# Kernel tuning notes

Hardware: AMD Instinct MI355X
Metric: run time of the kernel (lower is better)

Reference implementation:

```python
import jax, jax.numpy as jnp
import numpy as np

MINIMUM_VALUE = -1e9  # C.MINIMUM_VALUE: large negative fill for masked positions


def setup_inputs() -> dict:
    key = jax.random.key(0)
    kq, kv, km, kw = jax.random.split(key, 4)
    B, N, H = 8, 2048, 1024
    query = jax.random.normal(kq, (B, N, H), dtype=jnp.float32)
    value = jax.random.normal(kv, (B, N, H), dtype=jnp.float32)
    mask = jax.random.randint(km, (B, N, N), 0, 2, dtype=jnp.int32)
    W = jax.random.normal(kw, (H, H), dtype=jnp.float32)
    return {"query": query, "value": value, "mask": mask, "W": W}


def reference(query, value, mask, W):
    # intermediate = query @ W           : B x M x H
    # e = relu(intermediate @ value^T)   : B x M x N
    e = jax.nn.relu(jnp.einsum("bmh,hk,bnk->bmn", query, W, value))
    attn_logits = jnp.where(mask > 0, e, MINIMUM_VALUE)
    attn = jax.nn.softmax(attn_logits, axis=-1)
    output = jnp.einsum("bmn,bnh->bmh", attn, value)
    return (output, attn)
```

## Files before the change

kernel.cpp:

```cpp
#include <hip/hip_runtime.h>


typedef _Float16 half8 __attribute__((ext_vector_type(8)));
typedef float f32x4 __attribute__((ext_vector_type(4)));
typedef unsigned short u16;
typedef unsigned int u32;

#define BATCH 8
#define SEQ   2048
#define HID   1024
#define MINV  (-1e9f)

#define AS1 __attribute__((address_space(1)))
#define AS3 __attribute__((address_space(3)))

__device__ __forceinline__ u16 h2u(_Float16 h) { return __builtin_bit_cast(u16, h); }

__device__ __forceinline__ u32 packhl(float x) {
    _Float16 h = (_Float16)x;
    _Float16 l = (_Float16)(x - (float)h);
    return (u32)h2u(h) | ((u32)h2u(l) << 16);
}

__device__ __forceinline__ void gload16(const char* g, AS3 char* l) {
    __builtin_amdgcn_global_load_lds((const AS1 void*)g, (AS3 void*)l, 16, 0, 0);
}

__global__ __launch_bounds__(256) void prep_v(const float* __restrict__ V,
                                              u16* __restrict__ Vp,
                                              u16* __restrict__ Vt)
{
    __shared__ __align__(16) u16 lt[64 * 72];
    const int b = blockIdx.z, n0 = blockIdx.y * 64, h0 = blockIdx.x * 64;
    const int t = threadIdx.x;
    const int r = t >> 4, c4 = (t & 15) * 4;
#pragma unroll
    for (int it = 0; it < 4; ++it) {
        const int rr = r + it * 16;
        const float4 x = *(const float4*)(V + ((size_t)b * SEQ + n0 + rr) * HID + h0 + c4);
        const float xs[4] = {x.x, x.y, x.z, x.w};
        u32 p[4];
#pragma unroll
        for (int e = 0; e < 4; ++e) {
            p[e] = packhl(xs[e]);
            lt[(c4 + e) * 72 + rr] = (u16)p[e];
        }
        const int g = (h0 + c4) >> 5, j = c4 & 31;
        u16* base = Vp + (((size_t)b * SEQ + n0 + rr) * 32 + g) * 64;
        *(uint2*)(base + j) = make_uint2((p[0] & 0xffffu) | (p[1] << 16),
                                         (p[2] & 0xffffu) | (p[3] << 16));
        *(uint2*)(base + 32 + j) = make_uint2((p[0] >> 16) | (p[1] & 0xffff0000u),
                                              (p[2] >> 16) | (p[3] & 0xffff0000u));
    }
    __syncthreads();
    const int hr = t >> 2, cc = (t & 3) * 2;
    uint4 v0 = *(const uint4*)&lt[hr * 72 + cc * 8];
    uint4 v1 = *(const uint4*)&lt[hr * 72 + cc * 8 + 8];
    u16* dst = Vt + ((size_t)b * HID + h0 + hr) * SEQ + n0 + cc * 8;
    *(uint4*)dst = v0;
    *(uint4*)(dst + 8) = v1;
}

__global__ __launch_bounds__(256) void prep_w(const float* __restrict__ W,
                                              u16* __restrict__ Wtp)
{
    __shared__ __align__(16) u32 lt[64 * 68];
    const int n0 = blockIdx.x * 64, k0 = blockIdx.y * 64;
    const int t = threadIdx.x;
    const int r = t >> 4, c4 = (t & 15) * 4;
#pragma unroll
    for (int it = 0; it < 4; ++it) {
        const int rr = r + it * 16;
        const float4 x = *(const float4*)(W + (size_t)(k0 + rr) * HID + n0 + c4);
        const float xs[4] = {x.x, x.y, x.z, x.w};
#pragma unroll
        for (int e = 0; e < 4; ++e) lt[(c4 + e) * 68 + rr] = packhl(xs[e]);
    }
    __syncthreads();
    const int n = t >> 2;
#pragma unroll
    for (int s = 0; s < 4; ++s) {
        const int ci = (t & 3) + s * 4;
        uint4 v = *(const uint4*)&lt[n * 68 + ci * 4];
        const int k = k0 + ci * 4;
        u16* base = Wtp + (((size_t)n0 + n) * 32 + (k >> 5)) * 64;
        const int j = k & 31;
        *(uint2*)(base + j) = make_uint2((v.x & 0xffffu) | (v.y << 16),
                                         (v.z & 0xffffu) | (v.w << 16));
        *(uint2*)(base + 32 + j) = make_uint2((v.x >> 16) | (v.y & 0xffff0000u),
                                              (v.z >> 16) | (v.w & 0xffff0000u));
    }
}

__global__ __launch_bounds__(256) void prep_q(const float* __restrict__ Q,
                                              u16* __restrict__ Qp)
{
    const size_t row = blockIdx.x;
    const int t = threadIdx.x;
    const float4 x = ((const float4*)(Q + row * HID))[t];
    const u32 p0 = packhl(x.x), p1 = packhl(x.y), p2 = packhl(x.z), p3 = packhl(x.w);
    const int k = t * 4;
    u16* base = Qp + (row * 32 + (k >> 5)) * 64;
    const int j = k & 31;
    *(uint2*)(base + j) = make_uint2((p0 & 0xffffu) | (p1 << 16),
                                     (p2 & 0xffffu) | (p3 << 16));
    *(uint2*)(base + 32 + j) = make_uint2((p0 >> 16) | (p1 & 0xffff0000u),
                                          (p2 >> 16) | (p3 & 0xffff0000u));
}

template <bool SPLIT>
__device__ __forceinline__ void cluster4x2(f32x4 (&acc)[8][4], int ib, int jb,
                                           const half8 (&ah)[4], const half8 (&al)[4],
                                           half8 bh0, half8 bl0, half8 bh1, half8 bl1)
{
#pragma unroll
    for (int f = 0; f < 4; ++f) {
#pragma unroll
        for (int jj = 0; jj < 2; ++jj) {
            const half8 bh = jj ? bh1 : bh0;
            const half8 bl = jj ? bl1 : bl0;
            f32x4 c = acc[ib + f][jb + jj];
            if constexpr (SPLIT) {
                c = __builtin_amdgcn_mfma_f32_16x16x32_f16(al[f], bh, c, 0, 0, 0);
                c = __builtin_amdgcn_mfma_f32_16x16x32_f16(ah[f], bl, c, 0, 0, 0);
                c = __builtin_amdgcn_mfma_f32_16x16x32_f16(ah[f], bh, c, 0, 0, 0);
            } else {
                c = __builtin_amdgcn_mfma_f32_16x16x32_f16(ah[f], bh, c, 0, 0, 0);
                c = __builtin_amdgcn_mfma_f32_16x16x32_f16(al[f], bl, c, 0, 0, 0);
            }
            acc[ib + f][jb + jj] = c;
        }
    }
}

#define SBAR() __builtin_amdgcn_sched_barrier(0)

template <int MODE, int ROT, int CUR>
__device__ __forceinline__ void kstep(
    const char* pAh, const char* pAl, const char* pBh, const char* pBl,
    AS3 char* lds,
    const char* __restrict__ Ab, const char* __restrict__ Bb,
    const u32 (&aoffs)[4], const u32 (&boffs)[4], const int (&dsto)[4],
    u32 kb, bool more, f32x4 (&acc)[8][4])
{
    constexpr bool SPLIT = (MODE != 3);
    constexpr int FH = (ROT == 0) ? 0 : 16384;
    constexpr int SH = 16384 - FH;
    constexpr int GF = (ROT == 0) ? 0 : 16384;
    constexpr int GS = 16384 - GF;
    constexpr int AQ1 = (ROT == 0) ? 0 : 4;
    constexpr int AQ2 = 4 - AQ1;
    constexpr int BQ1 = (ROT == 0) ? 0 : 2;
    constexpr int BQ2 = 2 - BQ1;
    AS3 char* ldsA = lds + (CUR ^ 1) * 65536;
    AS3 char* ldsB = ldsA + 32768;

    asm volatile("s_waitcnt vmcnt(0)" ::: "memory");
    __builtin_amdgcn_s_barrier();
    SBAR();

    half8 ah[4], al[4];
#pragma unroll
    for (int i = 0; i < 4; ++i) {
        const int off = FH + (i >> 1) * 8192 + (i & 1) * 2048;
        ah[i] = *(const half8*)(pAh + off);
        al[i] = *(const half8*)(pAl + off);
    }
    half8 bFh0 = *(const half8*)(pBh + GF);
    half8 bFl0 = *(const half8*)(pBl + GF);
    half8 bFh1 = *(const half8*)(pBh + GF + 2048);
    half8 bFl1 = *(const half8*)(pBl + GF + 2048);
    if (more) {
#pragma unroll
        for (int it = 0; it < 4; ++it) gload16(Ab + (aoffs[it] + kb), ldsA + dsto[it]);
#pragma unroll
        for (int it = 0; it < 4; ++it) gload16(Bb + (boffs[it] + kb), ldsB + dsto[it]);
    }
    half8 bSh0 = *(const half8*)(pBh + GS);
    half8 bSl0 = *(const half8*)(pBl + GS);
    half8 bSh1 = *(const half8*)(pBh + GS + 2048);
    half8 bSl1 = *(const half8*)(pBl + GS + 2048);

    asm volatile("s_waitcnt lgkmcnt(4)" ::: "memory");
    SBAR();
    __builtin_amdgcn_s_setprio(1);
    cluster4x2<SPLIT>(acc, AQ1, BQ1, ah, al, bFh0, bFl0, bFh1, bFl1);
    __builtin_amdgcn_s_setprio(0);

    asm volatile("s_waitcnt lgkmcnt(0)" ::: "memory");
    SBAR();
    __builtin_amdgcn_s_setprio(1);
    cluster4x2<SPLIT>(acc, AQ1, BQ2, ah, al, bSh0, bSl0, bSh1, bSl1);
    __builtin_amdgcn_s_setprio(0);

#pragma unroll
    for (int i = 0; i < 4; ++i) {
        const int off = SH + (i >> 1) * 8192 + (i & 1) * 2048;
        ah[i] = *(const half8*)(pAh + off);
        al[i] = *(const half8*)(pAl + off);
    }
    asm volatile("s_waitcnt lgkmcnt(0)" ::: "memory");
    SBAR();
    __builtin_amdgcn_s_setprio(1);
    cluster4x2<SPLIT>(acc, AQ2, BQ2, ah, al, bSh0, bSl0, bSh1, bSl1);
    cluster4x2<SPLIT>(acc, AQ2, BQ1, ah, al, bFh0, bFl0, bFh1, bFl1);
    __builtin_amdgcn_s_setprio(0);
    SBAR();
}

template <int MODE, int ROT>
__device__ __forceinline__ void kloop(
    char* smem, const char* __restrict__ Ab, const char* __restrict__ Bb,
    const u32 (&aoffs)[4], const u32 (&boffs)[4], const int (&dsto)[4],
    int baseAhi, int baseAlo, int baseBhi, int baseBlo, f32x4 (&acc)[8][4])
{
    AS3 char* lds = (AS3 char*)smem;
    const char* pA0h = smem + baseAhi;
    const char* pA0l = smem + baseAlo;
    const char* pB0h = smem + baseBhi;
    const char* pB0l = smem + baseBlo;
    const char* pA1h = pA0h + 65536;
    const char* pA1l = pA0l + 65536;
    const char* pB1h = pB0h + 65536;
    const char* pB1l = pB0l + 65536;

    for (int ks = 0; ks < 32; ks += 2) {
        const u32 kb0 = (u32)(ks + 1) * 128u;
        const u32 kb1 = (u32)(ks + 2) * 128u;
        kstep<MODE, ROT, 0>(pA0h, pA0l, pB0h, pB0l, lds, Ab, Bb,
                            aoffs, boffs, dsto, kb0, true, acc);
        kstep<MODE, ROT, 1>(pA1h, pA1l, pB1h, pB1l, lds, Ab, Bb,
                            aoffs, boffs, dsto, kb1, ks < 30, acc);
    }
}

template <int MODE>
__device__ __forceinline__ void gemm_body(
    char* smem,
    const char* __restrict__ Abase, const char* __restrict__ Bbase,
    void* __restrict__ Cbase, const int* __restrict__ Mbase,
    int ldc, long sAb, long sBb, long sC, long sM)
{
    const int nx = gridDim.x, ny = gridDim.y;
    const int nxy = nx * ny;
    int wg = blockIdx.x + nx * (blockIdx.y + ny * blockIdx.z);
    const int cpx = (nxy * gridDim.z) >> 3;
    wg = (wg & 7) * cpx + (wg >> 3);
    const int bz = wg / nxy;
    const int rem = wg - bz * nxy;
    const int m0 = (rem / nx) * 256, n0 = (rem % nx) * 256;

    const int tid = threadIdx.x;
    const int w = tid >> 6, l = tid & 63;
    const int wm = w >> 2, wn = w & 3;
    const int lm = l & 15, q = l >> 4;

    const char* Ab = Abase + (long)bz * sAb;
    const char* Bb = Bbase + (long)bz * sBb;

    u32 aoffs[4], boffs[4];
    int dsto[4];
#pragma unroll
    for (int it = 0; it < 4; ++it) {
        const int off = it * 8192 + tid * 16;
        dsto[it] = off;
        const int row = off >> 7;
        const int swi = (off & 127) ^ ((row & 7) << 4);
        aoffs[it] = (u32)(m0 + row) * 4096u + (u32)swi;
        boffs[it] = (u32)(n0 + row) * 4096u + (u32)swi;
    }
    const int wofs = (q * 16) ^ ((lm & 7) << 4);
    const int baseAhi = (wm * 32 + lm) * 128 + wofs;
    const int baseAlo = (wm * 32 + lm) * 128 + (wofs ^ 64);
    const int baseBhi = 32768 + (wn * 32 + lm) * 128 + wofs;
    const int baseBlo = 32768 + (wn * 32 + lm) * 128 + (wofs ^ 64);

    f32x4 acc[8][4];
#pragma unroll
    for (int i = 0; i < 8; ++i)
#pragma unroll
        for (int j = 0; j < 4; ++j) acc[i][j] = (f32x4){0.f, 0.f, 0.f, 0.f};

    AS3 char* lds = (AS3 char*)smem;

#pragma unroll
    for (int it = 0; it < 4; ++it) gload16(Ab + aoffs[it], lds + dsto[it]);
#pragma unroll
    for (int it = 0; it < 4; ++it) gload16(Bb + boffs[it], lds + 32768 + dsto[it]);

    if (((w >> 2) & 1) == 0)
        kloop<MODE, 0>(smem, Ab, Bb, aoffs, boffs, dsto,
                       baseAhi, baseAlo, baseBhi, baseBlo, acc);
    else
        kloop<MODE, 1>(smem, Ab, Bb, aoffs, boffs, dsto,
                       baseAhi, baseAlo, baseBhi, baseBlo, acc);

#pragma unroll
    for (int i = 0; i < 8; ++i) {
        const int arow = (i >> 1) * 64 + wm * 32 + (i & 1) * 16 + q * 4;
#pragma unroll
        for (int r = 0; r < 4; ++r) {
            const int grow = m0 + arow + r;
#pragma unroll
            for (int j = 0; j < 4; ++j) {
                const int gcol = n0 + (j >> 1) * 128 + wn * 32 + (j & 1) * 16 + lm;
                const float v = acc[i][j][r];
                if constexpr (MODE == 1) {
                    const u32 p = packhl(v);
                    u16* base = (u16*)Cbase + ((size_t)grow * (ldc >> 5) + (gcol >> 5)) * 64;
                    base[gcol & 31] = (u16)p;
                    base[32 + (gcol & 31)] = (u16)(p >> 16);
                } else if constexpr (MODE == 2) {
                    const int mv = Mbase[(long)bz * sM + (long)grow * ldc + gcol];
                    ((float*)Cbase)[(long)bz * sC + (long)grow * ldc + gcol] =
                        (mv > 0) ? fmaxf(v, 0.f) : MINV;
                } else {
                    ((float*)Cbase)[(long)bz * sC + (long)grow * ldc + gcol] = v;
                }
            }
        }
    }
}

__global__ __launch_bounds__(512, 2) void gemm1_qw(
    const char* __restrict__ A, const char* __restrict__ B, void* __restrict__ C,
    const int* __restrict__ M, int ldc, long sAb, long sBb, long sC, long sM)
{
    extern __shared__ __align__(16) char smem[];
    gemm_body<1>(smem, A, B, C, M, ldc, sAb, sBb, sC, sM);
}
__global__ __launch_bounds__(512, 2) void gemm2_av(
    const char* __restrict__ A, const char* __restrict__ B, void* __restrict__ C,
    const int* __restrict__ M, int ldc, long sAb, long sBb, long sC, long sM)
{
    extern __shared__ __align__(16) char smem[];
    gemm_body<2>(smem, A, B, C, M, ldc, sAb, sBb, sC, sM);
}
__global__ __launch_bounds__(512, 2) void gemm3_out(
    const char* __restrict__ A, const char* __restrict__ B, void* __restrict__ C,
    const int* __restrict__ M, int ldc, long sAb, long sBb, long sC, long sM)
{
    extern __shared__ __align__(16) char smem[];
    gemm_body<3>(smem, A, B, C, M, ldc, sAb, sBb, sC, sM);
}

__global__ __launch_bounds__(256) void softmax2048(float* __restrict__ attn,
                                                   u16* __restrict__ attnH)
{
    const long row = blockIdx.x;
    float* p = attn + row * 2048;
    const int tid = threadIdx.x;

    float4 v0 = ((const float4*)p)[tid];
    float4 v1 = ((const float4*)p)[tid + 256];

    float mx = fmaxf(fmaxf(fmaxf(v0.x, v0.y), fmaxf(v0.z, v0.w)),
                     fmaxf(fmaxf(v1.x, v1.y), fmaxf(v1.z, v1.w)));
#pragma unroll
    for (int o = 32; o >= 1; o >>= 1)
        mx = fmaxf(mx, __shfl_xor(mx, o, 64));

    __shared__ float redm[4];
    __shared__ float reds[4];
    const int wid = tid >> 6, lane = tid & 63;
    if (lane == 0) redm[wid] = mx;
    __syncthreads();
    mx = fmaxf(fmaxf(redm[0], redm[1]), fmaxf(redm[2], redm[3]));

    float e[8];
    e[0] = __expf(v0.x - mx); e[1] = __expf(v0.y - mx);
    e[2] = __expf(v0.z - mx); e[3] = __expf(v0.w - mx);
    e[4] = __expf(v1.x - mx); e[5] = __expf(v1.y - mx);
    e[6] = __expf(v1.z - mx); e[7] = __expf(v1.w - mx);

    float s = ((e[0] + e[1]) + (e[2] + e[3])) + ((e[4] + e[5]) + (e[6] + e[7]));
#pragma unroll
    for (int o = 32; o >= 1; o >>= 1)
        s += __shfl_xor(s, o, 64);
    if (lane == 0) reds[wid] = s;
    __syncthreads();
    s = (reds[0] + reds[1]) + (reds[2] + reds[3]);

    const float inv = 1.0f / s;
    float o0 = e[0] * inv, o1 = e[1] * inv, o2 = e[2] * inv, o3 = e[3] * inv;
    float o4 = e[4] * inv, o5 = e[5] * inv, o6 = e[6] * inv, o7 = e[7] * inv;
    ((float4*)p)[tid]       = make_float4(o0, o1, o2, o3);
    ((float4*)p)[tid + 256] = make_float4(o4, o5, o6, o7);

    u16* ph = attnH + row * 2048;
    ((uint2*)ph)[tid] =
        make_uint2((u32)h2u((_Float16)o0) | ((u32)h2u((_Float16)o1) << 16),
                   (u32)h2u((_Float16)o2) | ((u32)h2u((_Float16)o3) << 16));
    ((uint2*)ph)[tid + 256] =
        make_uint2((u32)h2u((_Float16)o4) | ((u32)h2u((_Float16)o5) << 16),
                   (u32)h2u((_Float16)o6) | ((u32)h2u((_Float16)o7) << 16));
}

extern "C" void kernel_launch(void* const* d_in, const int* in_sizes, int n_in,
                              void* d_out, int out_size, void* d_ws, size_t ws_size,
                              hipStream_t stream)
{
    (void)in_sizes; (void)n_in; (void)out_size; (void)ws_size;

    const float* query = (const float*)d_in[0];
    const float* value = (const float*)d_in[1];
    const int*   mask  = (const int*)d_in[2];
    const float* W     = (const float*)d_in[3];

    float* out  = (float*)d_out;
    float* attn = out + (size_t)BATCH * SEQ * HID;

    u16* Vp  = (u16*)d_ws;
    u16* Vt  = (u16*)((char*)d_ws + ((size_t)64 << 20));
    u16* Wtp = (u16*)((char*)d_ws + ((size_t)96 << 20));

    u16* interP = (u16*)d_out;
    u16* Qp     = (u16*)attn;
    u16* attnH  = Vp;

    static int attr_done = 0;
    if (!attr_done) {
        hipFuncSetAttribute((const void*)gemm1_qw,
                            hipFuncAttributeMaxDynamicSharedMemorySize, 131072);
        hipFuncSetAttribute((const void*)gemm2_av,
                            hipFuncAttributeMaxDynamicSharedMemorySize, 131072);
        hipFuncSetAttribute((const void*)gemm3_out,
                            hipFuncAttributeMaxDynamicSharedMemorySize, 131072);
        attr_done = 1;
    }

    prep_v<<<dim3(HID / 64, SEQ / 64, BATCH), 256, 0, stream>>>(value, Vp, Vt);
    prep_w<<<dim3(HID / 64, HID / 64, 1), 256, 0, stream>>>(W, Wtp);
    prep_q<<<dim3(BATCH * SEQ), 256, 0, stream>>>(query, Qp);

    gemm1_qw<<<dim3(HID / 256, (BATCH * SEQ) / 256, 1), 512, 131072, stream>>>(
        (const char*)Qp, (const char*)Wtp, interP, nullptr,
        HID, 0, 0, 0, 0);

    gemm2_av<<<dim3(SEQ / 256, SEQ / 256, BATCH), 512, 131072, stream>>>(
        (const char*)interP, (const char*)Vp, attn, mask,
        SEQ, (long)SEQ * 4096, (long)SEQ * 4096, (long)SEQ * SEQ, (long)SEQ * SEQ);

    softmax2048<<<dim3(BATCH * SEQ), 256, 0, stream>>>(attn, attnH);

    gemm3_out<<<dim3(HID / 256, SEQ / 256, BATCH), 512, 131072, stream>>>(
        (const char*)attnH, (const char*)Vt, out, nullptr,
        HID, (long)SEQ * 4096, (long)HID * 4096, (long)SEQ * HID, 0);
}
```

Baseline: 715.9 us.

## Switch GEMM inner tiles from 16x16x32 to 32x32x16 MFMA with new wave mapping

Replaces the 16x16x32 f16 MFMA clusters with 32x32x16 MFMA tiles. Each wave now owns a 128x64 block held as 4x2 32x32 accumulators, and the LDS fragment addressing and epilogue row/column mapping are reworked to match. The change also drops the per-wave rotation of k-halves and the kloop wrapper. Larger MFMA tiles cut LDS fragment reads per FLOP and issue fewer instructions, at the risk of new LDS bank conflicts and a less coalesced epilogue store.

```diff
diff --git a/kernel.cpp b/kernel.cpp
--- a/kernel.cpp
+++ b/kernel.cpp
@@ -2,7 +2,7 @@
 
 
 typedef _Float16 half8 __attribute__((ext_vector_type(8)));
-typedef float f32x4 __attribute__((ext_vector_type(4)));
+typedef float f32x16 __attribute__((ext_vector_type(16)));
 typedef unsigned short u16;
 typedef unsigned int u32;
 
@@ -109,129 +109,86 @@
 }
 
 template <bool SPLIT>
-__device__ __forceinline__ void cluster4x2(f32x4 (&acc)[8][4], int ib, int jb,
-                                           const half8 (&ah)[4], const half8 (&al)[4],
-                                           half8 bh0, half8 bl0, half8 bh1, half8 bl1)
-{
-#pragma unroll
-    for (int f = 0; f < 4; ++f) {
-#pragma unroll
-        for (int jj = 0; jj < 2; ++jj) {
-            const half8 bh = jj ? bh1 : bh0;
-            const half8 bl = jj ? bl1 : bl0;
-            f32x4 c = acc[ib + f][jb + jj];
-            if constexpr (SPLIT) {
-                c = __builtin_amdgcn_mfma_f32_16x16x32_f16(al[f], bh, c, 0, 0, 0);
-                c = __builtin_amdgcn_mfma_f32_16x16x32_f16(ah[f], bl, c, 0, 0, 0);
-                c = __builtin_amdgcn_mfma_f32_16x16x32_f16(ah[f], bh, c, 0, 0, 0);
-            } else {
-                c = __builtin_amdgcn_mfma_f32_16x16x32_f16(ah[f], bh, c, 0, 0, 0);
-                c = __builtin_amdgcn_mfma_f32_16x16x32_f16(al[f], bl, c, 0, 0, 0);
-            }
-            acc[ib + f][jb + jj] = c;
+__device__ __forceinline__ void tilemm(f32x16& x, const half8 (&a)[4], const half8 (&b)[4])
+{
+    if constexpr (SPLIT) {
+#pragma unroll
+        for (int s = 0; s < 2; ++s) {
+            x = __builtin_amdgcn_mfma_f32_32x32x16_f16(a[s + 2], b[s], x, 0, 0, 0);
+            x = __builtin_amdgcn_mfma_f32_32x32x16_f16(a[s], b[s + 2], x, 0, 0, 0);
+            x = __builtin_amdgcn_mfma_f32_32x32x16_f16(a[s], b[s], x, 0, 0, 0);
         }
+    } else {
+#pragma unroll
+        for (int s = 0; s < 4; ++s)
+            x = __builtin_amdgcn_mfma_f32_32x32x16_f16(a[s], b[s], x, 0, 0, 0);
     }
 }
 
 #define SBAR() __builtin_amdgcn_sched_barrier(0)
 
-template <int MODE, int ROT, int CUR>
+template <int MODE>
 __device__ __forceinline__ void kstep(
-    const char* pAh, const char* pAl, const char* pBh, const char* pBl,
-    AS3 char* lds,
+    const char* pa, const char* pb, const int (&ko)[4],
+    AS3 char* ldsA, AS3 char* ldsB,
     const char* __restrict__ Ab, const char* __restrict__ Bb,
     const u32 (&aoffs)[4], const u32 (&boffs)[4], const int (&dsto)[4],
-    u32 kb, bool more, f32x4 (&acc)[8][4])
+    u32 kb, bool more, f32x16 (&acc)[4][2])
 {
     constexpr bool SPLIT = (MODE != 3);
-    constexpr int FH = (ROT == 0) ? 0 : 16384;
-    constexpr int SH = 16384 - FH;
-    constexpr int GF = (ROT == 0) ? 0 : 16384;
-    constexpr int GS = 16384 - GF;
-    constexpr int AQ1 = (ROT == 0) ? 0 : 4;
-    constexpr int AQ2 = 4 - AQ1;
-    constexpr int BQ1 = (ROT == 0) ? 0 : 2;
-    constexpr int BQ2 = 2 - BQ1;
-    AS3 char* ldsA = lds + (CUR ^ 1) * 65536;
-    AS3 char* ldsB = ldsA + 32768;
 
     asm volatile("s_waitcnt vmcnt(0)" ::: "memory");
     __builtin_amdgcn_s_barrier();
     SBAR();
 
-    half8 ah[4], al[4];
-#pragma unroll
-    for (int i = 0; i < 4; ++i) {
-        const int off = FH + (i >> 1) * 8192 + (i & 1) * 2048;
-        ah[i] = *(const half8*)(pAh + off);
-        al[i] = *(const half8*)(pAl + off);
-    }
-    half8 bFh0 = *(const half8*)(pBh + GF);
-    half8 bFl0 = *(const half8*)(pBl + GF);
-    half8 bFh1 = *(const half8*)(pBh + GF + 2048);
-    half8 bFl1 = *(const half8*)(pBl + GF + 2048);
+    half8 aF[2][4], bG[2][4];
+#pragma unroll
+    for (int t = 0; t < 2; ++t)
+#pragma unroll
+        for (int k = 0; k < 4; ++k)
+            aF[t][k] = *(const half8*)(pa + t * 4096 + ko[k]);
+#pragma unroll
+    for (int k = 0; k < 4; ++k)
+        bG[0][k] = *(const half8*)(pb + ko[k]);
     if (more) {
 #pragma unroll
         for (int it = 0; it < 4; ++it) gload16(Ab + (aoffs[it] + kb), ldsA + dsto[it]);
 #pragma unroll
         for (int it = 0; it < 4; ++it) gload16(Bb + (boffs[it] + kb), ldsB + dsto[it]);
     }
-    half8 bSh0 = *(const half8*)(pBh + GS);
-    half8 bSl0 = *(const half8*)(pBl + GS);
-    half8 bSh1 = *(const half8*)(pBh + GS + 2048);
-    half8 bSl1 = *(const half8*)(pBl + GS + 2048);
+#pragma unroll
+    for (int k = 0; k < 4; ++k)
+        bG[1][k] = *(const half8*)(pb + 4096 + ko[k]);
 
     asm volatile("s_waitcnt lgkmcnt(4)" ::: "memory");
     SBAR();
     __builtin_amdgcn_s_setprio(1);
-    cluster4x2<SPLIT>(acc, AQ1, BQ1, ah, al, bFh0, bFl0, bFh1, bFl1);
+    tilemm<SPLIT>(acc[0][0], aF[0], bG[0]);
+    tilemm<SPLIT>(acc[1][0], aF[1], bG[0]);
     __builtin_amdgcn_s_setprio(0);
 
     asm volatile("s_waitcnt lgkmcnt(0)" ::: "memory");
     SBAR();
     __builtin_amdgcn_s_setprio(1);
-    cluster4x2<SPLIT>(acc, AQ1, BQ2, ah, al, bSh0, bSl0, bSh1, bSl1);
+    tilemm<SPLIT>(acc[0][1], aF[0], bG[1]);
+    tilemm<SPLIT>(acc[1][1], aF[1], bG[1]);
     __builtin_amdgcn_s_setprio(0);
 
 #pragma unroll
-    for (int i = 0; i < 4; ++i) {
-        const int off = SH + (i >> 1) * 8192 + (i & 1) * 2048;
-        ah[i] = *(const half8*)(pAh + off);
-        al[i] = *(const half8*)(pAl + off);
-    }
+    for (int t = 0; t < 2; ++t)
+#pragma unroll
+        for (int k = 0; k < 4; ++k)
+            aF[t][k] = *(const half8*)(pa + 8192 + t * 4096 + ko[k]);
+
     asm volatile("s_waitcnt lgkmcnt(0)" ::: "memory");
     SBAR();
     __builtin_amdgcn_s_setprio(1);
-    cluster4x2<SPLIT>(acc, AQ2, BQ2, ah, al, bSh0, bSl0, bSh1, bSl1);
-    cluster4x2<SPLIT>(acc, AQ2, BQ1, ah, al, bFh0, bFl0, bFh1, bFl1);
+    tilemm<SPLIT>(acc[2][1], aF[0], bG[1]);
+    tilemm<SPLIT>(acc[3][1], aF[1], bG[1]);
+    tilemm<SPLIT>(acc[2][0], aF[0], bG[0]);
+    tilemm<SPLIT>(acc[3][0], aF[1], bG[0]);
     __builtin_amdgcn_s_setprio(0);
     SBAR();
-}
-
-template <int MODE, int ROT>
-__device__ __forceinline__ void kloop(
-    char* smem, const char* __restrict__ Ab, const char* __restrict__ Bb,
-    const u32 (&aoffs)[4], const u32 (&boffs)[4], const int (&dsto)[4],
-    int baseAhi, int baseAlo, int baseBhi, int baseBlo, f32x4 (&acc)[8][4])
-{
-    AS3 char* lds = (AS3 char*)smem;
-    const char* pA0h = smem + baseAhi;
-    const char* pA0l = smem + baseAlo;
-    const char* pB0h = smem + baseBhi;
-    const char* pB0l = smem + baseBlo;
-    const char* pA1h = pA0h + 65536;
-    const char* pA1l = pA0l + 65536;
-    const char* pB1h = pB0h + 65536;
-    const char* pB1l = pB0l + 65536;
-
-    for (int ks = 0; ks < 32; ks += 2) {
-        const u32 kb0 = (u32)(ks + 1) * 128u;
-        const u32 kb1 = (u32)(ks + 2) * 128u;
-        kstep<MODE, ROT, 0>(pA0h, pA0l, pB0h, pB0l, lds, Ab, Bb,
-                            aoffs, boffs, dsto, kb0, true, acc);
-        kstep<MODE, ROT, 1>(pA1h, pA1l, pB1h, pB1l, lds, Ab, Bb,
-                            aoffs, boffs, dsto, kb1, ks < 30, acc);
-    }
 }
 
 template <int MODE>
@@ -253,7 +210,7 @@
     const int tid = threadIdx.x;
     const int w = tid >> 6, l = tid & 63;
     const int wm = w >> 2, wn = w & 3;
-    const int lm = l & 15, q = l >> 4;
+    const int l31 = l & 31, q2 = l >> 5;
 
     const char* Ab = Abase + (long)bz * sAb;
     const char* Bb = Bbase + (long)bz * sBb;
@@ -269,17 +226,16 @@
         aoffs[it] = (u32)(m0 + row) * 4096u + (u32)swi;
         boffs[it] = (u32)(n0 + row) * 4096u + (u32)swi;
     }
-    const int wofs = (q * 16) ^ ((lm & 7) << 4);
-    const int baseAhi = (wm * 32 + lm) * 128 + wofs;
-    const int baseAlo = (wm * 32 + lm) * 128 + (wofs ^ 64);
-    const int baseBhi = 32768 + (wn * 32 + lm) * 128 + wofs;
-    const int baseBlo = 32768 + (wn * 32 + lm) * 128 + (wofs ^ 64);
-
-    f32x4 acc[8][4];
-#pragma unroll
-    for (int i = 0; i < 8; ++i)
-#pragma unroll
-        for (int j = 0; j < 4; ++j) acc[i][j] = (f32x4){0.f, 0.f, 0.f, 0.f};
+    const int kb16 = (q2 << 4) ^ ((l & 7) << 4);
+    int ko[4];
+#pragma unroll
+    for (int k = 0; k < 4; ++k) ko[k] = kb16 ^ (k << 5);
+
+    f32x16 acc[4][2];
+#pragma unroll
+    for (int i = 0; i < 4; ++i)
+#pragma unroll
+        for (int j = 0; j < 2; ++j) acc[i][j] = (f32x16)(0.f);
 
     AS3 char* lds = (AS3 char*)smem;
 
@@ -288,28 +244,38 @@
 #pragma unroll
     for (int it = 0; it < 4; ++it) gload16(Bb + boffs[it], lds + 32768 + dsto[it]);
 
-    if (((w >> 2) & 1) == 0)
-        kloop<MODE, 0>(smem, Ab, Bb, aoffs, boffs, dsto,
-                       baseAhi, baseAlo, baseBhi, baseBlo, acc);
-    else
-        kloop<MODE, 1>(smem, Ab, Bb, aoffs, boffs, dsto,
-                       baseAhi, baseAlo, baseBhi, baseBlo, acc);
-
-#pragma unroll
-    for (int i = 0; i < 8; ++i) {
-        const int arow = (i >> 1) * 64 + wm * 32 + (i & 1) * 16 + q * 4;
-#pragma unroll
-        for (int r = 0; r < 4; ++r) {
-            const int grow = m0 + arow + r;
-#pragma unroll
-            for (int j = 0; j < 4; ++j) {
-                const int gcol = n0 + (j >> 1) * 128 + wn * 32 + (j & 1) * 16 + lm;
-                const float v = acc[i][j][r];
+    const char* pa0 = smem + (wm * 128 + l31) * 128;
+    const char* pb0 = smem + 32768 + (wn * 64 + l31) * 128;
+    const char* pa1 = pa0 + 65536;
+    const char* pb1 = pb0 + 65536;
+    AS3 char* ldsA0 = lds;
+    AS3 char* ldsB0 = lds + 32768;
+    AS3 char* ldsA1 = lds + 65536;
+    AS3 char* ldsB1 = lds + 65536 + 32768;
+
+    for (int ks = 0; ks < 32; ks += 2) {
+        kstep<MODE>(pa0, pb0, ko, ldsA1, ldsB1, Ab, Bb, aoffs, boffs, dsto,
+                    (u32)(ks + 1) * 128u, true, acc);
+        kstep<MODE>(pa1, pb1, ko, ldsA0, ldsB0, Ab, Bb, aoffs, boffs, dsto,
+                    (u32)(ks + 2) * 128u, ks < 30, acc);
+    }
+
+#pragma unroll
+    for (int ti = 0; ti < 4; ++ti) {
+#pragma unroll
+        for (int ci = 0; ci < 2; ++ci) {
+            const int colbase = n0 + wn * 64 + ci * 32;
+#pragma unroll
+            for (int r = 0; r < 16; ++r) {
+                const int row = (r & 3) + 8 * (r >> 2) + 4 * q2;
+                const int grow = m0 + wm * 128 + ti * 32 + row;
+                const int gcol = colbase + l31;
+                const float v = acc[ti][ci][r];
                 if constexpr (MODE == 1) {
                     const u32 p = packhl(v);
-                    u16* base = (u16*)Cbase + ((size_t)grow * (ldc >> 5) + (gcol >> 5)) * 64;
-                    base[gcol & 31] = (u16)p;
-                    base[32 + (gcol & 31)] = (u16)(p >> 16);
+                    u16* base = (u16*)Cbase + ((size_t)grow * (ldc >> 5) + (colbase >> 5)) * 64;
+                    base[l31] = (u16)p;
+                    base[32 + l31] = (u16)(p >> 16);
                 } else if constexpr (MODE == 2) {
                     const int mv = Mbase[(long)bz * sM + (long)grow * ldc + gcol];
                     ((float*)Cbase)[(long)bz * sC + (long)grow * ldc + gcol] =
```

Result: slower. 745.2 us (+4.1%).
